# Optimization experiments

Hardware: AMD Instinct MI355X
Metric: run time of the kernel (lower is better)

The kernel has to match this reference:

```python
import jax, jax.numpy as jnp
import numpy as np

N_NODES = 100000
N_EDGES = 1600000
IN_DIM = 300
HID = 128
N_CLASSES = 3
N_ASPECTS = 2048


def setup_inputs() -> dict:
    key = jax.random.key(0)
    ks = jax.random.split(key, 8)
    features = jax.random.normal(ks[0], (N_NODES, IN_DIM), dtype=jnp.float32)
    edge_index = jax.random.randint(ks[1], (2, N_EDGES), 0, N_NODES, dtype=jnp.int64)
    aspect_indices = jax.random.randint(ks[2], (N_ASPECTS,), 0, N_NODES, dtype=jnp.int64)
    W1 = jax.random.normal(ks[3], (IN_DIM, HID), dtype=jnp.float32) * (1.0 / np.sqrt(IN_DIM))
    b1 = jnp.zeros((HID,), dtype=jnp.float32)
    W2 = jax.random.normal(ks[4], (HID, HID), dtype=jnp.float32) * (1.0 / np.sqrt(HID))
    b2 = jnp.zeros((HID,), dtype=jnp.float32)
    Wc = jax.random.normal(ks[5], (HID, N_CLASSES), dtype=jnp.float32) * (1.0 / np.sqrt(HID))
    bc = jnp.zeros((N_CLASSES,), dtype=jnp.float32)
    return {"features": features, "edge_index": edge_index, "aspect_indices": aspect_indices,
            "W1": W1, "b1": b1, "W2": W2, "b2": b2, "Wc": Wc, "bc": bc}


def _gcn_norm(edge_index, num_nodes):
    # PyG GCNConv: add self-loops, symmetric normalization D^-1/2 (A+I) D^-1/2
    loop = jnp.arange(num_nodes, dtype=edge_index.dtype)
    src = jnp.concatenate([edge_index[0], loop])
    dst = jnp.concatenate([edge_index[1], loop])
    deg = jax.ops.segment_sum(jnp.ones_like(dst, dtype=jnp.float32), dst,
                              num_segments=num_nodes)
    deg_inv_sqrt = jnp.where(deg > 0, jax.lax.rsqrt(deg), 0.0)
    norm = deg_inv_sqrt[src] * deg_inv_sqrt[dst]  # [E + N]
    return src, dst, norm


def _gcn_conv(x, src, dst, norm, W, b, num_nodes):
    h = x @ W                            # transform first (dim reduction)
    msg = h[src] * norm[:, None]         # gather + scale  [E+N, HID]
    out = jax.ops.segment_sum(msg, dst, num_segments=num_nodes)  # scatter-add
    return out + b


def reference(features, edge_index, aspect_indices, W1, b1, W2, b2, Wc, bc):
    num_nodes = features.shape[0]
    src, dst, norm = _gcn_norm(edge_index, num_nodes)
    h = _gcn_conv(features, src, dst, norm, W1, b1, num_nodes)
    h = jax.nn.relu(h)
    # dropout(p=0.3) -> identity in eval mode
    h = _gcn_conv(h, src, dst, norm, W2, b2, num_nodes)
    aspect_embeddings = h[aspect_indices]          # [N_ASPECTS, HID]
    logits = aspect_embeddings @ Wc + bc           # [N_ASPECTS, 3]
    return logits
```

## Files before the change

### kernel.cpp

```cpp
#include <hip/hip_runtime.h>

constexpr int NN = 100000;
constexpr int NE = 1600000;
constexpr int IN_DIM = 300;
constexpr int HID = 128;
constexpr int NA = 2048;
constexpr int NF_CAP = 50000;
constexpr int G1T = 1563;
constexpr int G1A = 782;
constexpr int G1B = G1T - G1A;
constexpr int EDGE_BLOCKS = 3125;

using short8 = __attribute__((ext_vector_type(8))) short;
using f32x4  = __attribute__((ext_vector_type(4))) float;

__device__ inline unsigned short f2bf(float x) {
    unsigned u = __float_as_uint(x);
    unsigned r = u + 0x7FFFu + ((u >> 16) & 1u);
    return (unsigned short)(r >> 16);
}
__device__ inline float bf2f(unsigned short h) {
    return __uint_as_float(((unsigned)h) << 16);
}

__device__ inline void gload_lds16(const void* g, void* l) {
    __builtin_amdgcn_global_load_lds(
        (const __attribute__((address_space(1))) unsigned int*)g,
        (__attribute__((address_space(3))) unsigned int*)l, 16, 0, 0);
}

__global__ void k_flag2(const int* __restrict__ asp, unsigned char* __restrict__ flags2,
                        int* __restrict__ flags1) {
    int i = blockIdx.x * blockDim.x + threadIdx.x;
    if (i < NA) {
        int n = asp[i];
        flags2[n] = 1;
        flags1[n] = 1;
    }
}

__global__ __launch_bounds__(1024) void k_scan2_local(const int* __restrict__ degi8,
                                                      const int* __restrict__ flags1,
                                                      int* __restrict__ off,
                                                      int* __restrict__ off2,
                                                      int* __restrict__ blksum,
                                                      int* __restrict__ blksum2,
                                                      float* __restrict__ dis) {
    __shared__ int sh[1024];
    __shared__ int sh2[1024];
    int t = threadIdx.x;
    int base = blockIdx.x * 1024;
    int ok = (base + t < NN);
    int f = ok ? flags1[base + t] : 0;
    int d = 0;
    if (ok) {
#pragma unroll
        for (int j = 0; j < 8; ++j) d += degi8[j * NN + base + t];
        dis[base + t] = rsqrtf((float)d + 1.0f);
    }
    int v = f ? d : 0;
    sh[t] = v;
    sh2[t] = f;
    __syncthreads();
    for (int s = 1; s < 1024; s <<= 1) {
        int a = (t >= s) ? sh[t - s] : 0;
        int a2 = (t >= s) ? sh2[t - s] : 0;
        __syncthreads();
        sh[t] += a;
        sh2[t] += a2;
        __syncthreads();
    }
    if (ok) {
        off[base + t] = sh[t] - v;
        off2[base + t] = sh2[t] - f;
    }
    if (t == 1023) {
        blksum[blockIdx.x] = sh[1023];
        blksum2[blockIdx.x] = sh2[1023];
    }
}

__global__ __launch_bounds__(128) void k_scan2_blk(int* __restrict__ blksum,
                                                   int* __restrict__ blksum2, int nb) {
    __shared__ int sh[128];
    __shared__ int sh2[128];
    int t = threadIdx.x;
    int v = (t < nb) ? blksum[t] : 0;
    int v2 = (t < nb) ? blksum2[t] : 0;
    sh[t] = v;
    sh2[t] = v2;
    __syncthreads();
    for (int s = 1; s < 128; s <<= 1) {
        int a = (t >= s) ? sh[t - s] : 0;
        int a2 = (t >= s) ? sh2[t - s] : 0;
        __syncthreads();
        sh[t] += a;
        sh2[t] += a2;
        __syncthreads();
    }
    if (t < nb) {
        blksum[t] = sh[t] - v;
        blksum2[t] = sh2[t] - v2;
    }
}

__global__ void k_scan2_add(int* __restrict__ off, int* __restrict__ off2,
                            const int* __restrict__ blksum, const int* __restrict__ blksum2,
                            const int* __restrict__ flags1,
                            int* __restrict__ list, int* __restrict__ remap,
                            int* __restrict__ nf) {
    int i = blockIdx.x * blockDim.x + threadIdx.x;
    if (i < NN) {
        off[i] += blksum[i >> 10];
        int o2 = off2[i] + blksum2[i >> 10];
        off2[i] = o2;
        int f = flags1[i];
        if (f && o2 < NF_CAP) {
            list[o2] = i;
            remap[i] = o2;
        }
        if (i == NN - 1) {
            int tot = o2 + f;
            *nf = (tot < NF_CAP) ? tot : NF_CAP;
        }
    }
}

__global__ void k_prepB(const float* __restrict__ B, unsigned short* __restrict__ img,
                        int K, int NT) {
    int i = blockIdx.x * blockDim.x + threadIdx.x;
    if (i >= NT * 4096) return;
    int kt = i >> 12;
    int rem = i & 4095;
    int ct = rem >> 9;
    int s = rem & 511;
    int lg = s >> 7;
    int lr = (s >> 3) & 15;
    int j = s & 7;
    int k = kt * 32 + lg * 8 + j;
    int col = ct * 16 + lr;
    float v = (k < K) ? B[k * 128 + col] : 0.f;
    unsigned short hi = f2bf(v);
    unsigned short lo = f2bf(v - bf2f(hi));
    img[kt * 8192 + ct * 1024 + s] = hi;
    img[kt * 8192 + ct * 1024 + 512 + s] = lo;
}

template <int K, int NT>
__device__ __forceinline__ void gemm_dev(int gbid, const float* __restrict__ A,
        const unsigned short* __restrict__ Bimg,
        float* __restrict__ C, int M, const int* __restrict__ Mptr) {
    __shared__ alignas(16) unsigned short ldsB[2][8192];
    const int Mv = Mptr ? *Mptr : M;
    const int row0 = gbid * 64;
    if (row0 >= Mv) return;
    const int t = threadIdx.x;
    const int w = t >> 6;
    const int l = t & 63;
    const int lr = l & 15;
    const int lg = l >> 4;
    const int wr = w & 3;
    const int wc = w >> 2;

    const int r0 = row0 + wr * 16 + lr;
    const long a0 = (long)(r0 < Mv ? r0 : Mv - 1) * K + lg * 8;

    f32x4 acc[4];
#pragma unroll
    for (int ct = 0; ct < 4; ++ct) acc[ct] = (f32x4){0.f, 0.f, 0.f, 0.f};

    float4 A0[2], A1[2];

    auto LOADA = [&](float4* buf, int kt) {
        const int k0 = kt * 32 + lg * 8;
        const float* s0 = A + a0 + kt * 32;
        if (k0 + 8 <= K) {
            buf[0] = *(const float4*)(s0);
            buf[1] = *(const float4*)(s0 + 4);
        } else {
            float t0[8];
#pragma unroll
            for (int j = 0; j < 8; ++j) t0[j] = (k0 + j < K) ? s0[j] : 0.f;
            buf[0] = make_float4(t0[0], t0[1], t0[2], t0[3]);
            buf[1] = make_float4(t0[4], t0[5], t0[6], t0[7]);
        }
    };

    auto STAGE_B = [&](int buf, int kt) {
        const char* g = (const char*)Bimg + (long)kt * 16384 + w * 2048 + l * 16;
        gload_lds16(g, &ldsB[buf][w * 1024]);
        gload_lds16(g + 1024, &ldsB[buf][w * 1024 + 512]);
    };

    auto CONV = [&](const float4* buf, short8& h0, short8& e0) {
        float v0[8] = {buf[0].x, buf[0].y, buf[0].z, buf[0].w, buf[1].x, buf[1].y, buf[1].z, buf[1].w};
#pragma unroll
        for (int j = 0; j < 8; ++j) {
            unsigned short hi = f2bf(v0[j]);
            h0[j] = (short)hi;
            e0[j] = (short)f2bf(v0[j] - bf2f(hi));
        }
    };

    auto COMPUTE = [&](const unsigned short* bbuf, short8 ah, short8 al) {
#pragma unroll
        for (int ct = 0; ct < 4; ++ct) {
            const unsigned short* bp = bbuf + (wc * 4 + ct) * 1024 + lg * 128 + lr * 8;
            short8 bh = *(const short8*)(bp);
            short8 bl = *(const short8*)(bp + 512);
            acc[ct] = __builtin_amdgcn_mfma_f32_16x16x32_bf16(ah, bh, acc[ct], 0, 0, 0);
            acc[ct] = __builtin_amdgcn_mfma_f32_16x16x32_bf16(al, bh, acc[ct], 0, 0, 0);
            acc[ct] = __builtin_amdgcn_mfma_f32_16x16x32_bf16(ah, bl, acc[ct], 0, 0, 0);
        }
    };

    LOADA(A0, 0);
    STAGE_B(0, 0);
    __syncthreads();
    for (int kt = 0; kt < NT; kt += 2) {
        if (kt + 1 < NT) {
            LOADA(A1, kt + 1);
            STAGE_B(1, kt + 1);
        }
        {
            short8 h0, e0;
            CONV(A0, h0, e0);
            COMPUTE(ldsB[0], h0, e0);
        }
        __syncthreads();
        if (kt + 1 < NT) {
            if (kt + 2 < NT) {
                LOADA(A0, kt + 2);
                STAGE_B(0, kt + 2);
            }
            short8 h0, e0;
            CONV(A1, h0, e0);
            COMPUTE(ldsB[1], h0, e0);
            __syncthreads();
        }
    }
#pragma unroll
    for (int ct = 0; ct < 4; ++ct)
#pragma unroll
        for (int r = 0; r < 4; ++r) {
            int row = row0 + wr * 16 + lg * 4 + r;
            if (row < Mv) C[(long)row * 128 + wc * 64 + ct * 16 + lr] = acc[ct][r];
        }
}

__global__ __launch_bounds__(512, 8) void k_fusedA(const float* __restrict__ A,
        const unsigned short* __restrict__ Bimg, float* __restrict__ C,
        const int* __restrict__ src, const int* __restrict__ dst,
        const unsigned char* __restrict__ flags2,
        int* __restrict__ degi8, int* __restrict__ flags1) {
    if (blockIdx.x < G1A) {
        gemm_dev<IN_DIM, 10>(blockIdx.x, A, Bimg, C, NN, nullptr);
    } else {
        int e = (blockIdx.x - G1A) * 512 + threadIdx.x;
        if (e < NE) {
            int d = dst[e];
            atomicAdd(&degi8[(blockIdx.x & 7) * NN + d], 1);
            if (flags2[d]) flags1[src[e]] = 1;
        }
    }
}

__global__ __launch_bounds__(512, 8) void k_fusedB(const float* __restrict__ A,
        const unsigned short* __restrict__ Bimg, float* __restrict__ C,
        const int* __restrict__ src, const int* __restrict__ dst,
        const int* __restrict__ flags1,
        int* __restrict__ off, int* __restrict__ csr) {
    if (blockIdx.x < G1B) {
        gemm_dev<IN_DIM, 10>(blockIdx.x + G1A, A, Bimg, C, NN, nullptr);
    } else {
        int e = (blockIdx.x - G1B) * 512 + threadIdx.x;
        if (e < NE) {
            int d = dst[e];
            if (flags1[d]) {
                int pos = atomicAdd(&off[d], 1);
                csr[pos] = src[e];
            }
        }
    }
}

__global__ __launch_bounds__(512, 8) void k_gemm2(const float* __restrict__ A,
        const unsigned short* __restrict__ Bimg, float* __restrict__ C,
        const int* __restrict__ nf) {
    gemm_dev<HID, 4>(blockIdx.x, A, Bimg, C, 0, nf);
}

__global__ __launch_bounds__(256) void k_gather1(const int* __restrict__ list,
                                                 const int* __restrict__ nf,
                                                 const int* __restrict__ csr,
                                                 const int* __restrict__ offpost,
                                                 const float* __restrict__ dis,
                                                 const float* __restrict__ h1,
                                                 const float* __restrict__ b1,
                                                 float* __restrict__ out) {
    int wave = threadIdx.x >> 6;
    int lane = threadIdx.x & 63;
    int half = lane >> 5;
    int sl = lane & 31;
    int idx = blockIdx.x * 4 + wave;
    if (idx >= *nf) return;
    int n = list[idx];
    int start = (n == 0) ? 0 : offpost[n - 1];
    int end = offpost[n];
    float dn = dis[n];
    float ax = 0.f, ay = 0.f, az = 0.f, aw = 0.f;
    int i = start + half;
    for (; i + 2 < end; i += 4) {
        int s0 = csr[i], s1 = csr[i + 2];
        float w0 = dis[s0], w1 = dis[s1];
        float4 v0 = *(const float4*)&h1[(long)s0 * HID + sl * 4];
        float4 v1 = *(const float4*)&h1[(long)s1 * HID + sl * 4];
        ax += w0 * v0.x + w1 * v1.x;
        ay += w0 * v0.y + w1 * v1.y;
        az += w0 * v0.z + w1 * v1.z;
        aw += w0 * v0.w + w1 * v1.w;
    }
    if (i < end) {
        int s = csr[i];
        float wgt = dis[s];
        float4 v = *(const float4*)&h1[(long)s * HID + sl * 4];
        ax += wgt * v.x;
        ay += wgt * v.y;
        az += wgt * v.z;
        aw += wgt * v.w;
    }
    ax += __shfl_xor(ax, 32);
    ay += __shfl_xor(ay, 32);
    az += __shfl_xor(az, 32);
    aw += __shfl_xor(aw, 32);
    if (half == 0) {
        float4 hv = *(const float4*)&h1[(long)n * HID + sl * 4];
        float4 bv = *(const float4*)&b1[sl * 4];
        float4 r;
        r.x = fmaxf(dn * (ax + dn * hv.x) + bv.x, 0.f);
        r.y = fmaxf(dn * (ay + dn * hv.y) + bv.y, 0.f);
        r.z = fmaxf(dn * (az + dn * hv.z) + bv.z, 0.f);
        r.w = fmaxf(dn * (aw + dn * hv.w) + bv.w, 0.f);
        *reinterpret_cast<float4*>(&out[(long)idx * HID + sl * 4]) = r;
    }
}

__global__ __launch_bounds__(256) void k_gather2(const int* __restrict__ asp,
                                                 const int* __restrict__ remap,
                                                 const int* __restrict__ csr,
                                                 const int* __restrict__ offpost,
                                                 const float* __restrict__ dis,
                                                 const float* __restrict__ t2,
                                                 const float* __restrict__ b2,
                                                 const float* __restrict__ Wc,
                                                 const float* __restrict__ bc,
                                                 float* __restrict__ out) {
    int wave = threadIdx.x >> 6;
    int lane = threadIdx.x & 63;
    int a = blockIdx.x * 4 + wave;
    if (a >= NA) return;
    int n = asp[a];
    int start = (n == 0) ? 0 : offpost[n - 1];
    int end = offpost[n];
    float dn = dis[n];
    float ax = 0.f, ay = 0.f;
    int i = start;
    for (; i + 4 <= end; i += 4) {
        int s0 = csr[i], s1 = csr[i + 1], s2 = csr[i + 2], s3 = csr[i + 3];
        float w0 = dis[s0], w1 = dis[s1], w2 = dis[s2], w3 = dis[s3];
        int r0 = remap[s0], r1 = remap[s1], r2 = remap[s2], r3 = remap[s3];
        float2 v0 = *(const float2*)&t2[(long)r0 * HID + lane * 2];
        float2 v1 = *(const float2*)&t2[(long)r1 * HID + lane * 2];
        float2 v2 = *(const float2*)&t2[(long)r2 * HID + lane * 2];
        float2 v3 = *(const float2*)&t2[(long)r3 * HID + lane * 2];
        ax += w0 * v0.x + w1 * v1.x + w2 * v2.x + w3 * v3.x;
        ay += w0 * v0.y + w1 * v1.y + w2 * v2.y + w3 * v3.y;
    }
    for (; i < end; ++i) {
        int s = csr[i];
        float w = dis[s];
        float2 v = *(const float2*)&t2[(long)remap[s] * HID + lane * 2];
        ax += w * v.x;
        ay += w * v.y;
    }
    float2 hv = *(const float2*)&t2[(long)remap[n] * HID + lane * 2];
    float vx = dn * (ax + dn * hv.x) + b2[2 * lane];
    float vy = dn * (ay + dn * hv.y) + b2[2 * lane + 1];
    float l0 = vx * Wc[(2 * lane) * 3 + 0] + vy * Wc[(2 * lane + 1) * 3 + 0];
    float l1 = vx * Wc[(2 * lane) * 3 + 1] + vy * Wc[(2 * lane + 1) * 3 + 1];
    float l2 = vx * Wc[(2 * lane) * 3 + 2] + vy * Wc[(2 * lane + 1) * 3 + 2];
#pragma unroll
    for (int s = 32; s > 0; s >>= 1) {
        l0 += __shfl_xor(l0, s);
        l1 += __shfl_xor(l1, s);
        l2 += __shfl_xor(l2, s);
    }
    if (lane == 0) {
        out[a * 3 + 0] = l0 + bc[0];
        out[a * 3 + 1] = l1 + bc[1];
        out[a * 3 + 2] = l2 + bc[2];
    }
}

extern "C" void kernel_launch(void* const* d_in, const int* in_sizes, int n_in,
                              void* d_out, int out_size, void* d_ws, size_t ws_size,
                              hipStream_t stream) {
    const float* features = (const float*)d_in[0];
    const int* ei = (const int*)d_in[1];
    const int* src = ei;
    const int* dst = ei + NE;
    const int* asp = (const int*)d_in[2];
    const float* W1 = (const float*)d_in[3];
    const float* b1 = (const float*)d_in[4];
    const float* W2 = (const float*)d_in[5];
    const float* b2 = (const float*)d_in[6];
    const float* Wc = (const float*)d_in[7];
    const float* bc = (const float*)d_in[8];
    float* out = (float*)d_out;

    char* ws = (char*)d_ws;
    float* dis   = (float*)(ws + 0);
    unsigned short* bimg1 = (unsigned short*)(ws + 400384);
    unsigned short* bimg2 = (unsigned short*)(ws + 400384 + 163840);
    int*   off   = (int*)  (ws + 800768);
    int*   blksum  = (int*)(ws + 1201152);
    int*   blksum2 = (int*)(ws + 1202176);
    int*   nf    = (int*)  (ws + 1203200);
    int*   csr   = (int*)  (ws + 1203328);
    int*   flags1= (int*)  (ws + 7603328);
    int*   off2  = (int*)  (ws + 8003328);
    int*   list  = (int*)  (ws + 8403328);
    int*   remap = (int*)  (ws + 8803328);
    float* bufA  = (float*)(ws + 9203328);
    float* bufB  = (float*)(ws + 60403328);
    int*   degi8 = (int*)  (ws + 60403328);
    unsigned char* flags2 = (unsigned char*)(ws + 86003328);

    const int NB = (NN + 1023) / 1024;

    hipMemsetAsync(degi8, 0, 8 * NN * sizeof(int), stream);
    hipMemsetAsync(flags1, 0, NN * sizeof(int), stream);
    hipMemsetAsync(flags2, 0, NN, stream);
    k_flag2<<<(NA + 255) / 256, 256, 0, stream>>>(asp, flags2, flags1);
    k_prepB<<<(10 * 4096 + 255) / 256, 256, 0, stream>>>(W1, bimg1, IN_DIM, 10);
    k_prepB<<<(4 * 4096 + 255) / 256, 256, 0, stream>>>(W2, bimg2, HID, 4);

    k_fusedA<<<G1A + EDGE_BLOCKS, 512, 0, stream>>>(
        features, bimg1, bufA, src, dst, flags2, degi8, flags1);

    k_scan2_local<<<NB, 1024, 0, stream>>>(degi8, flags1, off, off2, blksum, blksum2, dis);
    k_scan2_blk<<<1, 128, 0, stream>>>(blksum, blksum2, NB);
    k_scan2_add<<<(NN + 255) / 256, 256, 0, stream>>>(off, off2, blksum, blksum2,
                                                      flags1, list, remap, nf);

    k_fusedB<<<G1B + EDGE_BLOCKS, 512, 0, stream>>>(
        features, bimg1, bufA, src, dst, flags1, off, csr);

    k_gather1<<<(NF_CAP + 3) / 4, 256, 0, stream>>>(list, nf, csr, off, dis, bufA, b1, bufB);

    k_gemm2<<<(NF_CAP + 63) / 64, 512, 0, stream>>>(bufB, bimg2, bufA, nf);
    k_gather2<<<(NA + 3) / 4, 256, 0, stream>>>(asp, remap, csr, off, dis, bufA, b2, Wc, bc, out);
}
```

Measured before the change: 204.0 us.

## Preload all A tiles into registers and stage B in multi-tile phases

The GEMM device routine now issues every A-row load for the whole K dimension into registers up front, instead of double-buffering one tile at a time. B is staged into a larger LDS buffer holding PH k-tiles per phase, which cuts the number of barriers. Launch bounds drop from 8 to 2 blocks per CU, allowing many more registers per thread so the preloaded A fits. The aim is more memory-level parallelism and fewer syncs, paid for with lower occupancy, higher register pressure and larger LDS use per block (80KB for layer 1, 64KB for layer 2).

Measured after the change: 215.1 us. 5.4% more time.

```diff
diff --git a/kernel.cpp b/kernel.cpp
--- a/kernel.cpp
+++ b/kernel.cpp
@@ -146,11 +146,13 @@
     img[kt * 8192 + ct * 1024 + 512 + s] = lo;
 }
 
-template <int K, int NT>
+template <int K, int NT, int PH>
 __device__ __forceinline__ void gemm_dev(int gbid, const float* __restrict__ A,
         const unsigned short* __restrict__ Bimg,
         float* __restrict__ C, int M, const int* __restrict__ Mptr) {
-    __shared__ alignas(16) unsigned short ldsB[2][8192];
+    __shared__ alignas(16) unsigned short ldsB[PH * 8192];
+    constexpr int NPH = NT / PH;
+    static_assert(NT % PH == 0, "NT % PH");
     const int Mv = Mptr ? *Mptr : M;
     const int row0 = gbid * 64;
     if (row0 >= Mv) return;
@@ -169,74 +171,65 @@
 #pragma unroll
     for (int ct = 0; ct < 4; ++ct) acc[ct] = (f32x4){0.f, 0.f, 0.f, 0.f};
 
-    float4 A0[2], A1[2];
-
-    auto LOADA = [&](float4* buf, int kt) {
+    auto STAGE_PH = [&](int ph) {
+#pragma unroll
+        for (int h = 0; h < PH; ++h) {
+            const char* g = (const char*)Bimg + (long)(ph * PH + h) * 16384 + w * 2048 + l * 16;
+            gload_lds16(g, &ldsB[h * 8192 + w * 1024]);
+            gload_lds16(g + 1024, &ldsB[h * 8192 + w * 1024 + 512]);
+        }
+    };
+
+    STAGE_PH(0);
+    __syncthreads();
+
+    float4 Ar[2 * NT];
+#pragma unroll
+    for (int kt = 0; kt < NT; ++kt) {
         const int k0 = kt * 32 + lg * 8;
         const float* s0 = A + a0 + kt * 32;
         if (k0 + 8 <= K) {
-            buf[0] = *(const float4*)(s0);
-            buf[1] = *(const float4*)(s0 + 4);
+            Ar[2 * kt]     = *(const float4*)(s0);
+            Ar[2 * kt + 1] = *(const float4*)(s0 + 4);
         } else {
             float t0[8];
 #pragma unroll
             for (int j = 0; j < 8; ++j) t0[j] = (k0 + j < K) ? s0[j] : 0.f;
-            buf[0] = make_float4(t0[0], t0[1], t0[2], t0[3]);
-            buf[1] = make_float4(t0[4], t0[5], t0[6], t0[7]);
-        }
-    };
-
-    auto STAGE_B = [&](int buf, int kt) {
-        const char* g = (const char*)Bimg + (long)kt * 16384 + w * 2048 + l * 16;
-        gload_lds16(g, &ldsB[buf][w * 1024]);
-        gload_lds16(g + 1024, &ldsB[buf][w * 1024 + 512]);
-    };
-
-    auto CONV = [&](const float4* buf, short8& h0, short8& e0) {
-        float v0[8] = {buf[0].x, buf[0].y, buf[0].z, buf[0].w, buf[1].x, buf[1].y, buf[1].z, buf[1].w};
-#pragma unroll
-        for (int j = 0; j < 8; ++j) {
-            unsigned short hi = f2bf(v0[j]);
-            h0[j] = (short)hi;
-            e0[j] = (short)f2bf(v0[j] - bf2f(hi));
-        }
-    };
-
-    auto COMPUTE = [&](const unsigned short* bbuf, short8 ah, short8 al) {
-#pragma unroll
-        for (int ct = 0; ct < 4; ++ct) {
-            const unsigned short* bp = bbuf + (wc * 4 + ct) * 1024 + lg * 128 + lr * 8;
-            short8 bh = *(const short8*)(bp);
-            short8 bl = *(const short8*)(bp + 512);
-            acc[ct] = __builtin_amdgcn_mfma_f32_16x16x32_bf16(ah, bh, acc[ct], 0, 0, 0);
-            acc[ct] = __builtin_amdgcn_mfma_f32_16x16x32_bf16(al, bh, acc[ct], 0, 0, 0);
-            acc[ct] = __builtin_amdgcn_mfma_f32_16x16x32_bf16(ah, bl, acc[ct], 0, 0, 0);
-        }
-    };
-
-    LOADA(A0, 0);
-    STAGE_B(0, 0);
-    __syncthreads();
-    for (int kt = 0; kt < NT; kt += 2) {
-        if (kt + 1 < NT) {
-            LOADA(A1, kt + 1);
-            STAGE_B(1, kt + 1);
-        }
-        {
-            short8 h0, e0;
-            CONV(A0, h0, e0);
-            COMPUTE(ldsB[0], h0, e0);
-        }
-        __syncthreads();
-        if (kt + 1 < NT) {
-            if (kt + 2 < NT) {
-                LOADA(A0, kt + 2);
-                STAGE_B(0, kt + 2);
+            Ar[2 * kt]     = make_float4(t0[0], t0[1], t0[2], t0[3]);
+            Ar[2 * kt + 1] = make_float4(t0[4], t0[5], t0[6], t0[7]);
+        }
+    }
+
+#pragma unroll
+    for (int ph = 0; ph < NPH; ++ph) {
+        if (ph > 0) {
+            __syncthreads();
+            STAGE_PH(ph);
+            __syncthreads();
+        }
+#pragma unroll
+        for (int kk = 0; kk < PH; ++kk) {
+            const int kt = ph * PH + kk;
+            short8 ah, al;
+            {
+                const float4 b0 = Ar[2 * kt], b1 = Ar[2 * kt + 1];
+                float v0[8] = {b0.x, b0.y, b0.z, b0.w, b1.x, b1.y, b1.z, b1.w};
+#pragma unroll
+                for (int j = 0; j < 8; ++j) {
+                    unsigned short hi = f2bf(v0[j]);
+                    ah[j] = (short)hi;
+                    al[j] = (short)f2bf(v0[j] - bf2f(hi));
+                }
             }
-            short8 h0, e0;
-            CONV(A1, h0, e0);
-            COMPUTE(ldsB[1], h0, e0);
-            __syncthreads();
+#pragma unroll
+            for (int ct = 0; ct < 4; ++ct) {
+                const unsigned short* bp = &ldsB[kk * 8192] + (wc * 4 + ct) * 1024 + lg * 128 + lr * 8;
+                short8 bh = *(const short8*)(bp);
+                short8 bl = *(const short8*)(bp + 512);
+                acc[ct] = __builtin_amdgcn_mfma_f32_16x16x32_bf16(ah, bh, acc[ct], 0, 0, 0);
+                acc[ct] = __builtin_amdgcn_mfma_f32_16x16x32_bf16(al, bh, acc[ct], 0, 0, 0);
+                acc[ct] = __builtin_amdgcn_mfma_f32_16x16x32_bf16(ah, bl, acc[ct], 0, 0, 0);
+            }
         }
     }
 #pragma unroll
@@ -248,13 +241,13 @@
         }
 }
 
-__global__ __launch_bounds__(512, 8) void k_fusedA(const float* __restrict__ A,
+__global__ __launch_bounds__(512, 2) void k_fusedA(const float* __restrict__ A,
         const unsigned short* __restrict__ Bimg, float* __restrict__ C,
         const int* __restrict__ src, const int* __restrict__ dst,
         const unsigned char* __restrict__ flags2,
         int* __restrict__ degi8, int* __restrict__ flags1) {
     if (blockIdx.x < G1A) {
-        gemm_dev<IN_DIM, 10>(blockIdx.x, A, Bimg, C, NN, nullptr);
+        gemm_dev<IN_DIM, 10, 5>(blockIdx.x, A, Bimg, C, NN, nullptr);
     } else {
         int e = (blockIdx.x - G1A) * 512 + threadIdx.x;
         if (e < NE) {
@@ -265,13 +258,13 @@
     }
 }
 
-__global__ __launch_bounds__(512, 8) void k_fusedB(const float* __restrict__ A,
+__global__ __launch_bounds__(512, 2) void k_fusedB(const float* __restrict__ A,
         const unsigned short* __restrict__ Bimg, float* __restrict__ C,
         const int* __restrict__ src, const int* __restrict__ dst,
         const int* __restrict__ flags1,
         int* __restrict__ off, int* __restrict__ csr) {
     if (blockIdx.x < G1B) {
-        gemm_dev<IN_DIM, 10>(blockIdx.x + G1A, A, Bimg, C, NN, nullptr);
+        gemm_dev<IN_DIM, 10, 5>(blockIdx.x + G1A, A, Bimg, C, NN, nullptr);
     } else {
         int e = (blockIdx.x - G1B) * 512 + threadIdx.x;
         if (e < NE) {
@@ -284,10 +277,10 @@
     }
 }
 
-__global__ __launch_bounds__(512, 8) void k_gemm2(const float* __restrict__ A,
+__global__ __launch_bounds__(512, 2) void k_gemm2(const float* __restrict__ A,
         const unsigned short* __restrict__ Bimg, float* __restrict__ C,
         const int* __restrict__ nf) {
-    gemm_dev<HID, 4>(blockIdx.x, A, Bimg, C, 0, nf);
+    gemm_dev<HID, 4, 4>(blockIdx.x, A, Bimg, C, 0, nf);
 }
 
 __global__ __launch_bounds__(256) void k_gather1(const int* __restrict__ list,
```
